# Kernel tuning notes

Measured on AMD Instinct MI355X. Metric: run time of the kernel, lower is better.

Reference implementation:

```python
import jax, jax.numpy as jnp
import numpy as np

KEY_DIM = 32
D = 128  # attn_ratio * key_dim
H = 8
DIM = 512
N = 1024
B = 16
EPS = 1e-5


def setup_inputs() -> dict:
    key = jax.random.key(0)
    ks = jax.random.split(key, 5)
    x = jax.random.normal(ks[0], (B, DIM, N), dtype=jnp.float32)
    # grouped Conv1d(dim -> H*(2*key_dim+d), k=1, groups=H): per-group weight [H, 192, 64]
    qkv_w = jax.random.normal(ks[1], (H, 2 * KEY_DIM + D, DIM // H), dtype=jnp.float32) * 0.05
    qkv_b = jax.random.normal(ks[2], (H, 2 * KEY_DIM + D), dtype=jnp.float32) * 0.02
    # proj Conv1d(d*H -> dim, k=1)
    proj_w = jax.random.normal(ks[3], (DIM, D * H), dtype=jnp.float32) * 0.03
    proj_b = jax.random.normal(ks[4], (DIM,), dtype=jnp.float32) * 0.02
    bn_gamma = jnp.ones((DIM,), dtype=jnp.float32)
    bn_beta = jnp.zeros((DIM,), dtype=jnp.float32)
    bn_mean = jnp.zeros((DIM,), dtype=jnp.float32)
    bn_var = jnp.ones((DIM,), dtype=jnp.float32)
    return {"x": x, "qkv_w": qkv_w, "qkv_b": qkv_b, "proj_w": proj_w,
            "proj_b": proj_b, "bn_gamma": bn_gamma, "bn_beta": bn_beta,
            "bn_mean": bn_mean, "bn_var": bn_var}


def reference(x, qkv_w, qkv_b, proj_w, proj_b, bn_gamma, bn_beta, bn_mean, bn_var):
    Bx, C, Nx = x.shape
    scale = KEY_DIM ** (-0.5)
    # grouped 1x1 conv: split channels into H groups of C//H
    xh = x.reshape(Bx, H, C // H, Nx)                      # [B,H,Cg,N]
    qkv = jnp.einsum('bhcn,hoc->bhon', xh, qkv_w) + qkv_b[None, :, :, None]
    q, k, v = jnp.split(qkv, [KEY_DIM, 2 * KEY_DIM], axis=2)  # [B,H,kd,N],[B,H,kd,N],[B,H,d,N]
    # attn[m,n] = sum_c q[c,m]*k[c,n]
    attn = jnp.einsum('bhcm,bhcn->bhmn', q, k) * scale      # [B,H,N,N]
    attn = jax.nn.softmax(attn, axis=-1)
    # out[d,m] = sum_n v[d,n]*attn[m,n]  (v @ attn^T)
    o = jnp.einsum('bhdn,bhmn->bhdm', v, attn)              # [B,H,d,N]
    o = o.reshape(Bx, H * D, Nx)
    # proj: ReLU -> 1x1 conv -> BatchNorm1d (inference mode)
    o = jax.nn.relu(o)
    o = jnp.einsum('bcn,oc->bon', o, proj_w) + proj_b[None, :, None]
    inv = bn_gamma / jnp.sqrt(bn_var + EPS)
    o = o * inv[None, :, None] + (bn_beta - bn_mean * inv)[None, :, None]
    return o
```

## Files before the change

### kernel.cpp

```cpp
#include <hip/hip_runtime.h>
#include <math.h>

typedef unsigned short u16;
typedef unsigned int u32;

#define Bb   16
#define Hh   8
#define KD   32
#define DV   128
#define DIM  512
#define Nn   1024
#define OQKV 192
#define SCALE2 0.25503490221320355f

typedef short bf16x8 __attribute__((ext_vector_type(8)));
typedef float f32x16 __attribute__((ext_vector_type(16)));

#define MFMA32(a, b, c) __builtin_amdgcn_mfma_f32_32x32x16_bf16(a, b, c, 0, 0, 0)

__device__ __forceinline__ float fexp2(float x) {
#if __has_builtin(__builtin_amdgcn_exp2f)
  return __builtin_amdgcn_exp2f(x);
#else
  return exp2f(x);
#endif
}

__device__ __forceinline__ u16 f2bf_rn(float f) {
  return (u16)((__float_as_uint(f) + 0x8000u) >> 16);
}
__device__ __forceinline__ u32 pkrn(float lo, float hi) {
  u32 a = __float_as_uint(lo) + 0x8000u;
  u32 b = __float_as_uint(hi) + 0x8000u;
  return __builtin_amdgcn_perm(b, a, 0x07060302);
}

__global__ __launch_bounds__(256) void qkv_kernel(
    const float* __restrict__ x, const float* __restrict__ w,
    const float* __restrict__ bias, u16* __restrict__ Qb,
    u16* __restrict__ Kb, u16* __restrict__ Vb) {
  const int nt = blockIdx.x, bh = blockIdx.y;
  const int b = bh >> 3, h = bh & 7;
  const int tid = threadIdx.x;
  const int wid = tid >> 6, lane = tid & 63;
  const int r32 = lane & 31, hh = lane >> 5;
  const int n0 = nt * 128;

  __shared__ __align__(16) u16 Ws[192 * 72];
  __shared__ __align__(16) u16 Xs[128 * 72];

  const float* wp = w + (size_t)h * OQKV * 64;
  #pragma unroll
  for (int i = 0; i < 12; ++i) {
    int idx = i * 256 + tid;
    int o = idx >> 4, c4 = (idx & 15) * 4;
    float4 wv = *(const float4*)&wp[o * 64 + c4];
    uint2 pk; pk.x = pkrn(wv.x, wv.y); pk.y = pkrn(wv.z, wv.w);
    *(uint2*)&Ws[o * 72 + c4] = pk;
  }
  const float* xp = x + ((size_t)b * DIM + h * 64) * Nn + n0;
  #pragma unroll
  for (int i = 0; i < 8; ++i) {
    int idx = i * 256 + tid;
    int c = idx >> 5, n4 = (idx & 31) * 4;
    float4 xv = *(const float4*)&xp[(size_t)c * Nn + n4];
    Xs[(n4 + 0) * 72 + c] = f2bf_rn(xv.x);
    Xs[(n4 + 1) * 72 + c] = f2bf_rn(xv.y);
    Xs[(n4 + 2) * 72 + c] = f2bf_rn(xv.z);
    Xs[(n4 + 3) * 72 + c] = f2bf_rn(xv.w);
  }
  __syncthreads();

  f32x16 acc[6];
  #pragma unroll
  for (int t = 0; t < 6; ++t)
    #pragma unroll
    for (int r = 0; r < 16; ++r) acc[t][r] = 0.0f;

  const int nw = wid * 32;
  #pragma unroll
  for (int k = 0; k < 4; ++k) {
    const int ko = k * 16 + hh * 8;
    bf16x8 xb = *(const bf16x8*)&Xs[(nw + r32) * 72 + ko];
    #pragma unroll
    for (int t = 0; t < 6; ++t) {
      bf16x8 wa = *(const bf16x8*)&Ws[(t * 32 + r32) * 72 + ko];
      acc[t] = MFMA32(wa, xb, acc[t]);
    }
  }

  const int n = n0 + nw + r32;
  const float* bp = bias + h * OQKV;
  #pragma unroll
  for (int t = 0; t < 6; ++t) {
    #pragma unroll
    for (int g = 0; g < 4; ++g) {
      const int ob = t * 32 + 8 * g + 4 * hh;
      float4 bv = *(const float4*)&bp[ob];
      float v0 = acc[t][4 * g + 0] + bv.x;
      float v1 = acc[t][4 * g + 1] + bv.y;
      float v2 = acc[t][4 * g + 2] + bv.z;
      float v3 = acc[t][4 * g + 3] + bv.w;
      if (t == 0) {
        uint2 pk;
        pk.x = pkrn(v0 * SCALE2, v1 * SCALE2);
        pk.y = pkrn(v2 * SCALE2, v3 * SCALE2);
        *(uint2*)&Qb[((size_t)bh * Nn + n) * 32 + ob] = pk;
      } else if (t == 1) {
        uint2 pk; pk.x = pkrn(v0, v1); pk.y = pkrn(v2, v3);
        *(uint2*)&Kb[((size_t)bh * Nn + n) * 32 + ob - 32] = pk;
      } else {
        const int d = ob - 64;
        Vb[((size_t)bh * DV + d + 0) * Nn + n] = f2bf_rn(v0);
        Vb[((size_t)bh * DV + d + 1) * Nn + n] = f2bf_rn(v1);
        Vb[((size_t)bh * DV + d + 2) * Nn + n] = f2bf_rn(v2);
        Vb[((size_t)bh * DV + d + 3) * Nn + n] = f2bf_rn(v3);
      }
    }
  }
}

__global__ __launch_bounds__(256) void attn_kernel(
    const u16* __restrict__ Qb, const u16* __restrict__ Kb,
    const u16* __restrict__ Vb, u16* __restrict__ Ot) {
  const int blk = blockIdx.x;
  const int xcd = blk & 7, j = blk >> 3;
  const int bh = (xcd << 4) | (j >> 3);
  const int mt = j & 7;
  const int tid = threadIdx.x;
  const int wid = tid >> 6, lane = tid & 63;
  const int r32 = lane & 31, hh = lane >> 5;
  const int mw = mt * 128 + wid * 32;

  __shared__ __align__(16) u16 Vs[2][128 * 72];

  const u16* qp = Qb + ((size_t)bh * Nn + mw + r32) * 32;
  const bf16x8 qb0 = *(const bf16x8*)&qp[hh * 8];
  const bf16x8 qb1 = *(const bf16x8*)&qp[16 + hh * 8];

  const u16* kbase = Kb + (size_t)bh * Nn * 32;
  const u16* vbase = Vb + (size_t)bh * DV * Nn;

  int sd[4], sn[4];
  #pragma unroll
  for (int i = 0; i < 4; ++i) {
    int idx = i * 256 + tid;
    sd[i] = idx >> 3; sn[i] = (idx & 7) * 8;
  }

  uint4 vreg[4];
  #pragma unroll
  for (int i = 0; i < 4; ++i)
    vreg[i] = *(const uint4*)&vbase[(size_t)sd[i] * Nn + sn[i]];
  #pragma unroll
  for (int i = 0; i < 4; ++i)
    *(uint4*)&Vs[0][sd[i] * 72 + sn[i]] = vreg[i];

  f32x16 o[4];
  #pragma unroll
  for (int t = 0; t < 4; ++t)
    #pragma unroll
    for (int r = 0; r < 16; ++r) o[t][r] = 0.0f;
  float lsum = 0.0f;

  for (int ch = 0; ch < 16; ++ch) {
    const int n0 = ch * 64;
    const int p = ch & 1;
    __syncthreads();

    if (ch < 15) {
      #pragma unroll
      for (int i = 0; i < 4; ++i)
        vreg[i] = *(const uint4*)&vbase[(size_t)sd[i] * Nn + n0 + 64 + sn[i]];
    }

    const u16* kp0 = kbase + (size_t)(n0 + r32) * 32;
    const u16* kp1 = kbase + (size_t)(n0 + 32 + r32) * 32;
    bf16x8 ka0 = *(const bf16x8*)&kp0[hh * 8];
    bf16x8 ka1 = *(const bf16x8*)&kp0[16 + hh * 8];
    bf16x8 ka2 = *(const bf16x8*)&kp1[hh * 8];
    bf16x8 ka3 = *(const bf16x8*)&kp1[16 + hh * 8];

    f32x16 c0, c1;
    #pragma unroll
    for (int r = 0; r < 16; ++r) { c0[r] = 0.0f; c1[r] = 0.0f; }
    c0 = MFMA32(ka0, qb0, c0);
    c0 = MFMA32(ka1, qb1, c0);
    c1 = MFMA32(ka2, qb0, c1);
    c1 = MFMA32(ka3, qb1, c1);

    float csum = 0.0f;
    #pragma unroll
    for (int r = 0; r < 16; ++r) { c0[r] = fexp2(c0[r]); csum += c0[r]; }
    #pragma unroll
    for (int r = 0; r < 16; ++r) { c1[r] = fexp2(c1[r]); csum += c1[r]; }
    lsum += csum;

    u32 Pk[16], Rk[16];
    #pragma unroll
    for (int g = 0; g < 4; ++g) {
      Pk[2 * g]     = pkrn(c0[4 * g + 0], c0[4 * g + 1]);
      Pk[2 * g + 1] = pkrn(c0[4 * g + 2], c0[4 * g + 3]);
      Pk[8 + 2 * g]     = pkrn(c1[4 * g + 0], c1[4 * g + 1]);
      Pk[8 + 2 * g + 1] = pkrn(c1[4 * g + 2], c1[4 * g + 3]);
    }
    #pragma unroll
    for (int i = 0; i < 16; ++i) Rk[i] = __shfl_xor(Pk[i], 32, 64);

    union { u32 d[4]; bf16x8 v; } pb[4];
    #pragma unroll
    for (int q = 0; q < 2; ++q) {
      const int base = 8 * q;
      pb[2 * q].d[0] = hh ? Rk[base + 2] : Pk[base + 0];
      pb[2 * q].d[1] = hh ? Rk[base + 3] : Pk[base + 1];
      pb[2 * q].d[2] = hh ? Pk[base + 2] : Rk[base + 0];
      pb[2 * q].d[3] = hh ? Pk[base + 3] : Rk[base + 1];
      pb[2 * q + 1].d[0] = hh ? Rk[base + 6] : Pk[base + 4];
      pb[2 * q + 1].d[1] = hh ? Rk[base + 7] : Pk[base + 5];
      pb[2 * q + 1].d[2] = hh ? Pk[base + 6] : Rk[base + 4];
      pb[2 * q + 1].d[3] = hh ? Pk[base + 7] : Rk[base + 5];
    }

    #pragma unroll
    for (int t = 0; t < 4; ++t) {
      const u16* vrow = &Vs[p][(t * 32 + r32) * 72];
      #pragma unroll
      for (int s = 0; s < 4; ++s) {
        bf16x8 va = *(const bf16x8*)&vrow[s * 16 + hh * 8];
        o[t] = MFMA32(va, pb[s].v, o[t]);
      }
    }

    if (ch < 15) {
      #pragma unroll
      for (int i = 0; i < 4; ++i)
        *(uint4*)&Vs[1 - p][sd[i] * 72 + sn[i]] = vreg[i];
    }
  }

  lsum += __shfl_xor(lsum, 32, 64);
  const float inv = 1.0f / lsum;
  const int m = mw + r32;
  const int b = bh >> 3, h = bh & 7;
  u16* obase = Ot + ((size_t)b * Nn + m) * 1024 + h * DV + 4 * hh;
  #pragma unroll
  for (int t = 0; t < 4; ++t) {
    #pragma unroll
    for (int g = 0; g < 4; ++g) {
      float v0 = fmaxf(o[t][4 * g + 0] * inv, 0.0f);
      float v1 = fmaxf(o[t][4 * g + 1] * inv, 0.0f);
      float v2 = fmaxf(o[t][4 * g + 2] * inv, 0.0f);
      float v3 = fmaxf(o[t][4 * g + 3] * inv, 0.0f);
      uint2 pk; pk.x = pkrn(v0, v1); pk.y = pkrn(v2, v3);
      *(uint2*)&obase[t * 32 + 8 * g] = pk;
    }
  }
}

__global__ __launch_bounds__(256) void proj_kernel(
    const u16* __restrict__ Ot, const float* __restrict__ pw,
    const float* __restrict__ pb, const float* __restrict__ bn_g,
    const float* __restrict__ bn_b, const float* __restrict__ bn_m,
    const float* __restrict__ bn_v, float* __restrict__ out) {
  const int blk = blockIdx.x;
  const int xcd = blk & 7, rr = blk >> 3;
  const int pairl = rr >> 2, oct = rr & 3;
  const int pair = xcd * 16 + pairl;
  const int b = pair >> 3, nt = pair & 7;
  const int n0 = nt * 128, oc0 = oct * 128;
  const int tid = threadIdx.x;
  const int wid = tid >> 6, lane = tid & 63;
  const int r32 = lane & 31, hh = lane >> 5;
  const int ocw = (wid >> 1) * 64, nw = (wid & 1) * 64;

  __shared__ __align__(16) u16 Ws[128 * 40];
  __shared__ __align__(16) u16 Os[128 * 40];

  f32x16 o[2][2];
  #pragma unroll
  for (int t = 0; t < 2; ++t)
    #pragma unroll
    for (int u = 0; u < 2; ++u)
      #pragma unroll
      for (int r = 0; r < 16; ++r) o[t][u][r] = 0.0f;

  for (int ic0 = 0; ic0 < 1024; ic0 += 32) {
    __syncthreads();
    #pragma unroll
    for (int i = 0; i < 4; ++i) {
      int idx = i * 256 + tid;
      int row = idx >> 3, icq = (idx & 7) * 4;
      float4 wv = *(const float4*)&pw[(size_t)(oc0 + row) * 1024 + ic0 + icq];
      uint2 pk; pk.x = pkrn(wv.x, wv.y); pk.y = pkrn(wv.z, wv.w);
      *(uint2*)&Ws[row * 40 + icq] = pk;
    }
    #pragma unroll
    for (int i = 0; i < 2; ++i) {
      int idx = i * 256 + tid;
      int row = idx >> 2, ic8 = (idx & 3) * 8;
      *(uint4*)&Os[row * 40 + ic8] =
          *(const uint4*)&Ot[((size_t)b * Nn + n0 + row) * 1024 + ic0 + ic8];
    }
    __syncthreads();

    #pragma unroll
    for (int s = 0; s < 2; ++s) {
      const int ko = s * 16 + hh * 8;
      bf16x8 a0 = *(const bf16x8*)&Ws[(ocw + r32) * 40 + ko];
      bf16x8 a1 = *(const bf16x8*)&Ws[(ocw + 32 + r32) * 40 + ko];
      bf16x8 b0 = *(const bf16x8*)&Os[(nw + r32) * 40 + ko];
      bf16x8 b1 = *(const bf16x8*)&Os[(nw + 32 + r32) * 40 + ko];
      o[0][0] = MFMA32(a0, b0, o[0][0]);
      o[0][1] = MFMA32(a0, b1, o[0][1]);
      o[1][0] = MFMA32(a1, b0, o[1][0]);
      o[1][1] = MFMA32(a1, b1, o[1][1]);
    }
  }

  #pragma unroll
  for (int t = 0; t < 2; ++t) {
    const int obase = oc0 + ocw + t * 32 + 4 * hh;
    #pragma unroll
    for (int g = 0; g < 4; ++g) {
      const int oc = obase + 8 * g;
      float4 gv = *(const float4*)&bn_g[oc];
      float4 vv = *(const float4*)&bn_v[oc];
      float4 bv = *(const float4*)&bn_b[oc];
      float4 mv = *(const float4*)&bn_m[oc];
      float4 pv = *(const float4*)&pb[oc];
      float inv4[4], add4[4];
      inv4[0] = gv.x * rsqrtf(vv.x + 1e-5f);
      inv4[1] = gv.y * rsqrtf(vv.y + 1e-5f);
      inv4[2] = gv.z * rsqrtf(vv.z + 1e-5f);
      inv4[3] = gv.w * rsqrtf(vv.w + 1e-5f);
      add4[0] = pv.x * inv4[0] + bv.x - mv.x * inv4[0];
      add4[1] = pv.y * inv4[1] + bv.y - mv.y * inv4[1];
      add4[2] = pv.z * inv4[2] + bv.z - mv.z * inv4[2];
      add4[3] = pv.w * inv4[3] + bv.w - mv.w * inv4[3];
      #pragma unroll
      for (int u = 0; u < 2; ++u) {
        const int n = n0 + nw + u * 32 + r32;
        #pragma unroll
        for (int i = 0; i < 4; ++i) {
          float val = o[t][u][4 * g + i] * inv4[i] + add4[i];
          out[((size_t)b * DIM + oc + i) * Nn + n] = val;
        }
      }
    }
  }
}

extern "C" void kernel_launch(void* const* d_in, const int* in_sizes, int n_in,
                              void* d_out, int out_size, void* d_ws,
                              size_t ws_size, hipStream_t stream) {
  const float* x      = (const float*)d_in[0];
  const float* qkv_w  = (const float*)d_in[1];
  const float* qkv_b  = (const float*)d_in[2];
  const float* proj_w = (const float*)d_in[3];
  const float* proj_b = (const float*)d_in[4];
  const float* bn_g   = (const float*)d_in[5];
  const float* bn_b   = (const float*)d_in[6];
  const float* bn_m   = (const float*)d_in[7];
  const float* bn_v   = (const float*)d_in[8];
  float* out = (float*)d_out;

  char* ws = (char*)d_ws;
  u16* Qb = (u16*)(ws);
  u16* Kb = (u16*)(ws + 8388608);
  u16* Vb = (u16*)(ws + 16777216);
  u16* Ot = (u16*)(ws + 50331648);

  qkv_kernel<<<dim3(8, Bb * Hh), 256, 0, stream>>>(x, qkv_w, qkv_b, Qb, Kb, Vb);
  attn_kernel<<<dim3(1024), 256, 0, stream>>>(Qb, Kb, Vb, Ot);
  proj_kernel<<<dim3(512), 256, 0, stream>>>(
      Ot, proj_w, proj_b, bn_g, bn_b, bn_m, bn_v, out);
}
```

Measured before the change: 220.3 us.

## Pre-convert weights to bf16, prefetch K tiles, widen proj K-step, use hardware bf16 pack

New measurement: 213.1 us. -3.3%, faster.

```diff
diff --git a/kernel.cpp b/kernel.cpp
--- a/kernel.cpp
+++ b/kernel.cpp
@@ -29,14 +29,46 @@
 __device__ __forceinline__ u16 f2bf_rn(float f) {
   return (u16)((__float_as_uint(f) + 0x8000u) >> 16);
 }
-__device__ __forceinline__ u32 pkrn(float lo, float hi) {
+
+#if __has_builtin(__builtin_amdgcn_cvt_pk_bf16_f32)
+__device__ __forceinline__ u32 pk2(float lo, float hi) {
+  auto r = __builtin_amdgcn_cvt_pk_bf16_f32(lo, hi);
+  return __builtin_bit_cast(u32, r);
+}
+#else
+__device__ __forceinline__ u32 pk2(float lo, float hi) {
   u32 a = __float_as_uint(lo) + 0x8000u;
   u32 b = __float_as_uint(hi) + 0x8000u;
   return __builtin_amdgcn_perm(b, a, 0x07060302);
 }
+#endif
+
+__global__ __launch_bounds__(256) void prep_kernel(
+    const float* __restrict__ pw, const float* __restrict__ qw,
+    const float* __restrict__ pb, const float* __restrict__ g,
+    const float* __restrict__ bt, const float* __restrict__ mn,
+    const float* __restrict__ vr, u16* __restrict__ Wb,
+    u16* __restrict__ Wq, float* __restrict__ invA, float* __restrict__ addB) {
+  const int tid = blockIdx.x * 256 + threadIdx.x;
+  {
+    float4 v = *(const float4*)&pw[(size_t)tid * 4];
+    uint2 pk; pk.x = pk2(v.x, v.y); pk.y = pk2(v.z, v.w);
+    *(uint2*)&Wb[(size_t)tid * 4] = pk;
+  }
+  if (tid < 24576) {
+    float4 v = *(const float4*)&qw[(size_t)tid * 4];
+    uint2 pk; pk.x = pk2(v.x, v.y); pk.y = pk2(v.z, v.w);
+    *(uint2*)&Wq[(size_t)tid * 4] = pk;
+  }
+  if (tid < DIM) {
+    float inv = g[tid] * rsqrtf(vr[tid] + 1e-5f);
+    invA[tid] = inv;
+    addB[tid] = pb[tid] * inv + bt[tid] - mn[tid] * inv;
+  }
+}
 
 __global__ __launch_bounds__(256) void qkv_kernel(
-    const float* __restrict__ x, const float* __restrict__ w,
+    const float* __restrict__ x, const u16* __restrict__ Wq,
     const float* __restrict__ bias, u16* __restrict__ Qb,
     u16* __restrict__ Kb, u16* __restrict__ Vb) {
   const int nt = blockIdx.x, bh = blockIdx.y;
@@ -49,25 +81,25 @@
   __shared__ __align__(16) u16 Ws[192 * 72];
   __shared__ __align__(16) u16 Xs[128 * 72];
 
-  const float* wp = w + (size_t)h * OQKV * 64;
-  #pragma unroll
-  for (int i = 0; i < 12; ++i) {
+  const u16* wqp = Wq + (size_t)h * OQKV * 64;
+  #pragma unroll
+  for (int i = 0; i < 6; ++i) {
     int idx = i * 256 + tid;
-    int o = idx >> 4, c4 = (idx & 15) * 4;
-    float4 wv = *(const float4*)&wp[o * 64 + c4];
-    uint2 pk; pk.x = pkrn(wv.x, wv.y); pk.y = pkrn(wv.z, wv.w);
-    *(uint2*)&Ws[o * 72 + c4] = pk;
+    int o = idx >> 3, c8 = (idx & 7) * 8;
+    *(uint4*)&Ws[o * 72 + c8] = *(const uint4*)&wqp[o * 64 + c8];
   }
   const float* xp = x + ((size_t)b * DIM + h * 64) * Nn + n0;
   #pragma unroll
-  for (int i = 0; i < 8; ++i) {
+  for (int i = 0; i < 4; ++i) {
     int idx = i * 256 + tid;
-    int c = idx >> 5, n4 = (idx & 31) * 4;
-    float4 xv = *(const float4*)&xp[(size_t)c * Nn + n4];
-    Xs[(n4 + 0) * 72 + c] = f2bf_rn(xv.x);
-    Xs[(n4 + 1) * 72 + c] = f2bf_rn(xv.y);
-    Xs[(n4 + 2) * 72 + c] = f2bf_rn(xv.z);
-    Xs[(n4 + 3) * 72 + c] = f2bf_rn(xv.w);
+    int cp = idx >> 5, n4 = (idx & 31) * 4;
+    const int c = 2 * cp;
+    float4 a = *(const float4*)&xp[(size_t)c * Nn + n4];
+    float4 d = *(const float4*)&xp[(size_t)(c + 1) * Nn + n4];
+    *(u32*)&Xs[(n4 + 0) * 72 + c] = pk2(a.x, d.x);
+    *(u32*)&Xs[(n4 + 1) * 72 + c] = pk2(a.y, d.y);
+    *(u32*)&Xs[(n4 + 2) * 72 + c] = pk2(a.z, d.z);
+    *(u32*)&Xs[(n4 + 3) * 72 + c] = pk2(a.w, d.w);
   }
   __syncthreads();
 
@@ -103,11 +135,11 @@
       float v3 = acc[t][4 * g + 3] + bv.w;
       if (t == 0) {
         uint2 pk;
-        pk.x = pkrn(v0 * SCALE2, v1 * SCALE2);
-        pk.y = pkrn(v2 * SCALE2, v3 * SCALE2);
+        pk.x = pk2(v0 * SCALE2, v1 * SCALE2);
+        pk.y = pk2(v2 * SCALE2, v3 * SCALE2);
         *(uint2*)&Qb[((size_t)bh * Nn + n) * 32 + ob] = pk;
       } else if (t == 1) {
-        uint2 pk; pk.x = pkrn(v0, v1); pk.y = pkrn(v2, v3);
+        uint2 pk; pk.x = pk2(v0, v1); pk.y = pk2(v2, v3);
         *(uint2*)&Kb[((size_t)bh * Nn + n) * 32 + ob - 32] = pk;
       } else {
         const int d = ob - 64;
@@ -156,6 +188,16 @@
   for (int i = 0; i < 4; ++i)
     *(uint4*)&Vs[0][sd[i] * 72 + sn[i]] = vreg[i];
 
+  bf16x8 ka[4];
+  {
+    const u16* kp0 = kbase + (size_t)r32 * 32;
+    const u16* kp1 = kbase + (size_t)(32 + r32) * 32;
+    ka[0] = *(const bf16x8*)&kp0[hh * 8];
+    ka[1] = *(const bf16x8*)&kp0[16 + hh * 8];
+    ka[2] = *(const bf16x8*)&kp1[hh * 8];
+    ka[3] = *(const bf16x8*)&kp1[16 + hh * 8];
+  }
+
   f32x16 o[4];
   #pragma unroll
   for (int t = 0; t < 4; ++t)
@@ -174,20 +216,23 @@
         vreg[i] = *(const uint4*)&vbase[(size_t)sd[i] * Nn + n0 + 64 + sn[i]];
     }
 
-    const u16* kp0 = kbase + (size_t)(n0 + r32) * 32;
-    const u16* kp1 = kbase + (size_t)(n0 + 32 + r32) * 32;
-    bf16x8 ka0 = *(const bf16x8*)&kp0[hh * 8];
-    bf16x8 ka1 = *(const bf16x8*)&kp0[16 + hh * 8];
-    bf16x8 ka2 = *(const bf16x8*)&kp1[hh * 8];
-    bf16x8 ka3 = *(const bf16x8*)&kp1[16 + hh * 8];
-
     f32x16 c0, c1;
     #pragma unroll
     for (int r = 0; r < 16; ++r) { c0[r] = 0.0f; c1[r] = 0.0f; }
-    c0 = MFMA32(ka0, qb0, c0);
-    c0 = MFMA32(ka1, qb1, c0);
-    c1 = MFMA32(ka2, qb0, c1);
-    c1 = MFMA32(ka3, qb1, c1);
+    c0 = MFMA32(ka[0], qb0, c0);
+    c0 = MFMA32(ka[1], qb1, c0);
+    c1 = MFMA32(ka[2], qb0, c1);
+    c1 = MFMA32(ka[3], qb1, c1);
+
+    bf16x8 kn[4];
+    if (ch < 15) {
+      const u16* kp0 = kbase + (size_t)(n0 + 64 + r32) * 32;
+      const u16* kp1 = kbase + (size_t)(n0 + 96 + r32) * 32;
+      kn[0] = *(const bf16x8*)&kp0[hh * 8];
+      kn[1] = *(const bf16x8*)&kp0[16 + hh * 8];
+      kn[2] = *(const bf16x8*)&kp1[hh * 8];
+      kn[3] = *(const bf16x8*)&kp1[16 + hh * 8];
+    }
 
     float csum = 0.0f;
     #pragma unroll
@@ -199,10 +244,10 @@
     u32 Pk[16], Rk[16];
     #pragma unroll
     for (int g = 0; g < 4; ++g) {
-      Pk[2 * g]     = pkrn(c0[4 * g + 0], c0[4 * g + 1]);
-      Pk[2 * g + 1] = pkrn(c0[4 * g + 2], c0[4 * g + 3]);
-      Pk[8 + 2 * g]     = pkrn(c1[4 * g + 0], c1[4 * g + 1]);
-      Pk[8 + 2 * g + 1] = pkrn(c1[4 * g + 2], c1[4 * g + 3]);
+      Pk[2 * g]     = pk2(c0[4 * g + 0], c0[4 * g + 1]);
+      Pk[2 * g + 1] = pk2(c0[4 * g + 2], c0[4 * g + 3]);
+      Pk[8 + 2 * g]     = pk2(c1[4 * g + 0], c1[4 * g + 1]);
+      Pk[8 + 2 * g + 1] = pk2(c1[4 * g + 2], c1[4 * g + 3]);
     }
     #pragma unroll
     for (int i = 0; i < 16; ++i) Rk[i] = __shfl_xor(Pk[i], 32, 64);
@@ -235,6 +280,8 @@
       #pragma unroll
       for (int i = 0; i < 4; ++i)
         *(uint4*)&Vs[1 - p][sd[i] * 72 + sn[i]] = vreg[i];
+      #pragma unroll
+      for (int i = 0; i < 4; ++i) ka[i] = kn[i];
     }
   }
 
@@ -251,17 +298,16 @@
       float v1 = fmaxf(o[t][4 * g + 1] * inv, 0.0f);
       float v2 = fmaxf(o[t][4 * g + 2] * inv, 0.0f);
       float v3 = fmaxf(o[t][4 * g + 3] * inv, 0.0f);
-      uint2 pk; pk.x = pkrn(v0, v1); pk.y = pkrn(v2, v3);
+      uint2 pk; pk.x = pk2(v0, v1); pk.y = pk2(v2, v3);
       *(uint2*)&obase[t * 32 + 8 * g] = pk;
     }
   }
 }
 
 __global__ __launch_bounds__(256) void proj_kernel(
-    const u16* __restrict__ Ot, const float* __restrict__ pw,
-    const float* __restrict__ pb, const float* __restrict__ bn_g,
-    const float* __restrict__ bn_b, const float* __restrict__ bn_m,
-    const float* __restrict__ bn_v, float* __restrict__ out) {
+    const u16* __restrict__ Ot, const u16* __restrict__ Wb,
+    const float* __restrict__ invA, const float* __restrict__ addB,
+    float* __restrict__ out) {
   const int blk = blockIdx.x;
   const int xcd = blk & 7, rr = blk >> 3;
   const int pairl = rr >> 2, oct = rr & 3;
@@ -273,8 +319,8 @@
   const int r32 = lane & 31, hh = lane >> 5;
   const int ocw = (wid >> 1) * 64, nw = (wid & 1) * 64;
 
-  __shared__ __align__(16) u16 Ws[128 * 40];
-  __shared__ __align__(16) u16 Os[128 * 40];
+  __shared__ __align__(16) u16 Ws[128 * 72];
+  __shared__ __align__(16) u16 Os[128 * 72];
 
   f32x16 o[2][2];
   #pragma unroll
@@ -284,32 +330,31 @@
       #pragma unroll
       for (int r = 0; r < 16; ++r) o[t][u][r] = 0.0f;
 
-  for (int ic0 = 0; ic0 < 1024; ic0 += 32) {
+  for (int ic0 = 0; ic0 < 1024; ic0 += 64) {
     __syncthreads();
     #pragma unroll
     for (int i = 0; i < 4; ++i) {
       int idx = i * 256 + tid;
-      int row = idx >> 3, icq = (idx & 7) * 4;
-      float4 wv = *(const float4*)&pw[(size_t)(oc0 + row) * 1024 + ic0 + icq];
-      uint2 pk; pk.x = pkrn(wv.x, wv.y); pk.y = pkrn(wv.z, wv.w);
-      *(uint2*)&Ws[row * 40 + icq] = pk;
-    }
-    #pragma unroll
-    for (int i = 0; i < 2; ++i) {
+      int row = idx >> 3, c8 = (idx & 7) * 8;
+      *(uint4*)&Ws[row * 72 + c8] =
+          *(const uint4*)&Wb[(size_t)(oc0 + row) * 1024 + ic0 + c8];
+    }
+    #pragma unroll
+    for (int i = 0; i < 4; ++i) {
       int idx = i * 256 + tid;
-      int row = idx >> 2, ic8 = (idx & 3) * 8;
-      *(uint4*)&Os[row * 40 + ic8] =
-          *(const uint4*)&Ot[((size_t)b * Nn + n0 + row) * 1024 + ic0 + ic8];
+      int row = idx >> 3, c8 = (idx & 7) * 8;
+      *(uint4*)&Os[row * 72 + c8] =
+          *(const uint4*)&Ot[((size_t)b * Nn + n0 + row) * 1024 + ic0 + c8];
     }
     __syncthreads();
 
     #pragma unroll
-    for (int s = 0; s < 2; ++s) {
+    for (int s = 0; s < 4; ++s) {
       const int ko = s * 16 + hh * 8;
-      bf16x8 a0 = *(const bf16x8*)&Ws[(ocw + r32) * 40 + ko];
-      bf16x8 a1 = *(const bf16x8*)&Ws[(ocw + 32 + r32) * 40 + ko];
-      bf16x8 b0 = *(const bf16x8*)&Os[(nw + r32) * 40 + ko];
-      bf16x8 b1 = *(const bf16x8*)&Os[(nw + 32 + r32) * 40 + ko];
+      bf16x8 a0 = *(const bf16x8*)&Ws[(ocw + r32) * 72 + ko];
+      bf16x8 a1 = *(const bf16x8*)&Ws[(ocw + 32 + r32) * 72 + ko];
+      bf16x8 b0 = *(const bf16x8*)&Os[(nw + r32) * 72 + ko];
+      bf16x8 b1 = *(const bf16x8*)&Os[(nw + 32 + r32) * 72 + ko];
       o[0][0] = MFMA32(a0, b0, o[0][0]);
       o[0][1] = MFMA32(a0, b1, o[0][1]);
       o[1][0] = MFMA32(a1, b0, o[1][0]);
@@ -323,28 +368,15 @@
     #pragma unroll
     for (int g = 0; g < 4; ++g) {
       const int oc = obase + 8 * g;
-      float4 gv = *(const float4*)&bn_g[oc];
-      float4 vv = *(const float4*)&bn_v[oc];
-      float4 bv = *(const float4*)&bn_b[oc];
-      float4 mv = *(const float4*)&bn_m[oc];
-      float4 pv = *(const float4*)&pb[oc];
-      float inv4[4], add4[4];
-      inv4[0] = gv.x * rsqrtf(vv.x + 1e-5f);
-      inv4[1] = gv.y * rsqrtf(vv.y + 1e-5f);
-      inv4[2] = gv.z * rsqrtf(vv.z + 1e-5f);
-      inv4[3] = gv.w * rsqrtf(vv.w + 1e-5f);
-      add4[0] = pv.x * inv4[0] + bv.x - mv.x * inv4[0];
-      add4[1] = pv.y * inv4[1] + bv.y - mv.y * inv4[1];
-      add4[2] = pv.z * inv4[2] + bv.z - mv.z * inv4[2];
-      add4[3] = pv.w * inv4[3] + bv.w - mv.w * inv4[3];
+      float4 iv = *(const float4*)&invA[oc];
+      float4 av = *(const float4*)&addB[oc];
       #pragma unroll
       for (int u = 0; u < 2; ++u) {
         const int n = n0 + nw + u * 32 + r32;
-        #pragma unroll
-        for (int i = 0; i < 4; ++i) {
-          float val = o[t][u][4 * g + i] * inv4[i] + add4[i];
-          out[((size_t)b * DIM + oc + i) * Nn + n] = val;
-        }
+        out[((size_t)b * DIM + oc + 0) * Nn + n] = o[t][u][4 * g + 0] * iv.x + av.x;
+        out[((size_t)b * DIM + oc + 1) * Nn + n] = o[t][u][4 * g + 1] * iv.y + av.y;
+        out[((size_t)b * DIM + oc + 2) * Nn + n] = o[t][u][4 * g + 2] * iv.z + av.z;
+        out[((size_t)b * DIM + oc + 3) * Nn + n] = o[t][u][4 * g + 3] * iv.w + av.w;
       }
     }
   }
@@ -365,13 +397,18 @@
   float* out = (float*)d_out;
 
   char* ws = (char*)d_ws;
-  u16* Qb = (u16*)(ws);
-  u16* Kb = (u16*)(ws + 8388608);
-  u16* Vb = (u16*)(ws + 16777216);
-  u16* Ot = (u16*)(ws + 50331648);
-
-  qkv_kernel<<<dim3(8, Bb * Hh), 256, 0, stream>>>(x, qkv_w, qkv_b, Qb, Kb, Vb);
+  u16* Qb   = (u16*)(ws);
+  u16* Kb   = (u16*)(ws + 8388608);
+  u16* Vb   = (u16*)(ws + 16777216);
+  u16* Ot   = (u16*)(ws + 50331648);
+  u16* Wb   = (u16*)(ws + 83886080);
+  u16* Wq   = (u16*)(ws + 84934656);
+  float* invA = (float*)(ws + 85131264);
+  float* addB = (float*)(ws + 85133312);
+
+  prep_kernel<<<dim3(512), 256, 0, stream>>>(
+      proj_w, qkv_w, proj_b, bn_g, bn_b, bn_m, bn_v, Wb, Wq, invA, addB);
+  qkv_kernel<<<dim3(8, Bb * Hh), 256, 0, stream>>>(x, Wq, qkv_b, Qb, Kb, Vb);
   attn_kernel<<<dim3(1024), 256, 0, stream>>>(Qb, Kb, Vb, Ot);
-  proj_kernel<<<dim3(512), 256, 0, stream>>>(
-      Ot, proj_w, proj_b, bn_g, bn_b, bn_m, bn_v, out);
-}
+  proj_kernel<<<dim3(512), 256, 0, stream>>>(Ot, Wb, invA, addB, out);
+}
```
